# Kernel tuning notes

Hardware: AMD Instinct MI355X
Metric: run time of the kernel (lower is better)

## Reference

```python
import jax, jax.numpy as jnp
import numpy as np

N_NODES, N_EDGES, NNZ, F_IN, HID, K = 50000, 10000, 800000, 128, 512, 10


def setup_inputs() -> dict:
    key = jax.random.key(0)
    ks = jax.random.split(key, 6)
    x = jax.random.normal(ks[0], (N_NODES, F_IN), dtype=jnp.float32)
    node_idx = jax.random.randint(ks[1], (NNZ,), 0, N_NODES)
    edge_idx = jax.random.randint(ks[2], (NNZ,), 0, N_EDGES)
    hyperedge_index = jnp.stack([node_idx, edge_idx]).astype(jnp.int64)
    edge_weight = jax.random.uniform(ks[3], (N_EDGES,), dtype=jnp.float32, minval=0.5, maxval=1.5)
    theta = jax.random.normal(ks[4], (K + 1,), dtype=jnp.float32) * 0.1
    lin1_w = jax.random.normal(ks[5], (HID, F_IN), dtype=jnp.float32) * (1.0 / np.sqrt(F_IN))
    lin1_b = jnp.zeros((HID,), dtype=jnp.float32)
    return {"x": x, "hyperedge_index": hyperedge_index, "edge_weight": edge_weight,
            "theta": theta, "lin1_w": lin1_w, "lin1_b": lin1_b}


def _hyper_prop_factory(node_idx, edge_idx, edge_weight, n_nodes, n_edges):
    """Returns A_norm @ x where A_norm = Dv^-1/2 H W De^-1 H^T Dv^-1/2."""
    ones = jnp.ones_like(node_idx, dtype=edge_weight.dtype)
    d_e = jax.ops.segment_sum(ones, edge_idx, num_segments=n_edges)            # edge degree
    d_v = jax.ops.segment_sum(edge_weight[edge_idx], node_idx, num_segments=n_nodes)
    dv_is = jnp.where(d_v > 0, jax.lax.rsqrt(jnp.maximum(d_v, 1e-12)), 0.0)
    de_w = edge_weight * jnp.where(d_e > 0, 1.0 / jnp.maximum(d_e, 1e-12), 0.0)

    def prop(x):
        xv = x * dv_is[:, None]                                               # [N, F]
        m_e = jax.ops.segment_sum(xv[node_idx], edge_idx, num_segments=n_edges)
        m_e = m_e * de_w[:, None]                                             # [E, F]
        out = jax.ops.segment_sum(m_e[edge_idx], node_idx, num_segments=n_nodes)
        return out * dv_is[:, None]

    return prop


def cheb_hypergraph(x, node_idx, edge_idx, edge_weight, theta, n_nodes, n_edges):
    # L_tilde = L - I = -A_norm (lambda_max = 2). Chebyshev recurrence on L_tilde.
    prop = _hyper_prop_factory(node_idx, edge_idx, edge_weight, n_nodes, n_edges)
    t_prev = x                       # T_0
    out = theta[0] * t_prev
    t_cur = -prop(x)                 # T_1 = L_tilde x
    out = out + theta[1] * t_cur
    for k in range(2, theta.shape[0]):
        t_next = -2.0 * prop(t_cur) - t_prev   # T_k = 2 L_tilde T_{k-1} - T_{k-2}
        out = out + theta[k] * t_next
        t_prev, t_cur = t_cur, t_next
    return out


def reference(x, hyperedge_index, edge_weight, theta, lin1_w, lin1_b):
    node_idx = hyperedge_index[0]
    edge_idx = hyperedge_index[1]
    n_nodes = x.shape[0]
    n_edges = edge_weight.shape[0]
    # eval mode: both dropouts are identity
    h = cheb_hypergraph(x, node_idx, edge_idx, edge_weight, theta, n_nodes, n_edges)
    h = jnp.einsum('nf,hf->nh', h, lin1_w) + lin1_b
    # is_bns=False -> no batch norm; act_fn='relu'
    return jax.nn.relu(h)
```

## Files before the change

### kernel.cpp

```cpp
#include <hip/hip_runtime.h>


#define N_NODES 50000
#define N_EDGES 10000
#define NNZ     800000
#define F_IN    128
#define HID     512
#define F4      (F_IN / 4)
#define R16     16
#define NB_E    10
#define NB_N    49

typedef __attribute__((ext_vector_type(8))) short bf16x8;
typedef __attribute__((ext_vector_type(4))) float f32x4;

static __device__ __forceinline__ unsigned short f2bf(float f) {
    union { float f; unsigned u; } c; c.f = f;
    unsigned u = c.u;
    unsigned r = (u + 0x7fffu + ((u >> 16) & 1u)) >> 16;
    return (unsigned short)r;
}
static __device__ __forceinline__ float blo(unsigned u) {
    union { unsigned u; float f; } c; c.u = u << 16; return c.f;
}
static __device__ __forceinline__ float bhi(unsigned u) {
    union { unsigned u; float f; } c; c.u = u & 0xffff0000u; return c.f;
}
static __device__ __forceinline__ unsigned pack2(float lo, float hi) {
    return (unsigned)f2bf(lo) | ((unsigned)f2bf(hi) << 16);
}

__global__ void k_zero8(int* __restrict__ cnt8_e, int* __restrict__ cnt8_n) {
    int i = blockIdx.x * blockDim.x + threadIdx.x;
    if (i < 8 * N_NODES) cnt8_n[i] = 0;
    if (i < 8 * N_EDGES) cnt8_e[i] = 0;
}

__global__ void k_degrees(const int* __restrict__ hidx,
                          int* __restrict__ cnt8_e,
                          int* __restrict__ cnt8_n,
                          int* __restrict__ rank_e,
                          int* __restrict__ rank_v) {
    int i = blockIdx.x * blockDim.x + threadIdx.x;
    if (i >= NNZ) return;
    int xcd = (int)blockIdx.x & 7;
    int v = hidx[i];
    int e = hidx[NNZ + i];
    v = min(max(v, 0), N_NODES - 1);
    e = min(max(e, 0), N_EDGES - 1);
    int re = atomicAdd(&cnt8_e[xcd * N_EDGES + e], 1);
    int rv = atomicAdd(&cnt8_n[xcd * N_NODES + v], 1);
    rank_e[i] = re | (xcd << 24);
    rank_v[i] = rv | (xcd << 24);
}

__global__ void k_off8(int* __restrict__ cnt8_e,
                       int* __restrict__ cnt8_n,
                       int* __restrict__ counts_e,
                       int* __restrict__ counts_n) {
    int i = blockIdx.x * blockDim.x + threadIdx.x;
    if (i < N_EDGES) {
        int s = 0;
#pragma unroll
        for (int x = 0; x < 8; ++x) {
            int c = cnt8_e[x * N_EDGES + i];
            cnt8_e[x * N_EDGES + i] = s;
            s += c;
        }
        counts_e[i] = s;
    }
    if (i < N_NODES) {
        int s = 0;
#pragma unroll
        for (int x = 0; x < 8; ++x) {
            int c = cnt8_n[x * N_NODES + i];
            cnt8_n[x * N_NODES + i] = s;
            s += c;
        }
        counts_n[i] = s;
    }
}

__global__ __launch_bounds__(1024) void k_scan_blk2(const int* __restrict__ ce,
                                                    const int* __restrict__ cn,
                                                    int* __restrict__ oute,
                                                    int* __restrict__ outn,
                                                    int* __restrict__ pe,
                                                    int* __restrict__ pn) {
    __shared__ int sd[1024];
    int b = (int)blockIdx.x;
    const int* counts; int n; int* out; int* partial; int lb;
    if (b < NB_E) { counts = ce; n = N_EDGES; out = oute; partial = pe; lb = b; }
    else          { counts = cn; n = N_NODES; out = outn; partial = pn; lb = b - NB_E; }
    int tid = (int)threadIdx.x;
    int i = lb * 1024 + tid;
    int v = (i < n) ? counts[i] : 0;
    sd[tid] = v;
    __syncthreads();
    for (int off = 1; off < 1024; off <<= 1) {
        int t = (tid >= off) ? sd[tid - off] : 0;
        __syncthreads();
        sd[tid] += t;
        __syncthreads();
    }
    if (i < n) out[i] = sd[tid] - v;
    if (tid == 1023) partial[lb] = sd[1023];
}

__global__ void k_scan_top2(int* __restrict__ pe, int* __restrict__ pn,
                            int* __restrict__ tot_e, int* __restrict__ tot_n) {
    int w = (int)threadIdx.x >> 6;
    int lane = (int)threadIdx.x & 63;
    int* partial = w ? pn : pe;
    int nb       = w ? NB_N : NB_E;
    int* total   = w ? tot_n : tot_e;
    int v = (lane < nb) ? partial[lane] : 0;
    int incl = v;
    for (int off = 1; off < 64; off <<= 1) {
        int t = __shfl_up(incl, off);
        if (lane >= off) incl += t;
    }
    if (lane < nb) partial[lane] = incl - v;
    if (lane == 63) *total = incl;
}

__global__ __launch_bounds__(1024) void k_scan_add2(int* __restrict__ oute,
                                                    int* __restrict__ outn,
                                                    const int* __restrict__ pe,
                                                    const int* __restrict__ pn) {
    int b = (int)blockIdx.x;
    int* out; const int* partial; int n; int lb;
    if (b < NB_E) { out = oute; partial = pe; n = N_EDGES; lb = b; }
    else          { out = outn; partial = pn; n = N_NODES; lb = b - NB_E; }
    int i = lb * 1024 + (int)threadIdx.x;
    if (i < n) out[i] += partial[lb];
}

__global__ void k_fill(const int* __restrict__ hidx,
                       const int* __restrict__ edge_ptr,
                       const int* __restrict__ node_ptr,
                       const int* __restrict__ rank_e,
                       const int* __restrict__ rank_v,
                       const int* __restrict__ off8_e,
                       const int* __restrict__ off8_n,
                       int* __restrict__ edge_node,
                       int* __restrict__ node_edge) {
    int i = blockIdx.x * blockDim.x + threadIdx.x;
    if (i >= NNZ) return;
    int v = hidx[i];
    int e = hidx[NNZ + i];
    v = min(max(v, 0), N_NODES - 1);
    e = min(max(e, 0), N_EDGES - 1);
    int pe = rank_e[i];
    int pv = rank_v[i];
    int xe = pe >> 24, re = pe & 0xFFFFFF;
    int xv = pv >> 24, rv = pv & 0xFFFFFF;
    edge_node[edge_ptr[e] + off8_e[xe * N_EDGES + e] + re] = v;
    node_edge[node_ptr[v] + off8_n[xv * N_NODES + v] + rv] = e;
}

__global__ void k_norms2(const float* __restrict__ ew,
                         const int* __restrict__ edge_ptr,
                         const int* __restrict__ node_ptr,
                         const int* __restrict__ node_edge,
                         float* __restrict__ dv_is,
                         float* __restrict__ de_w) {
    int i = blockIdx.x * blockDim.x + threadIdx.x;
    if (i < N_NODES) {
        int s = node_ptr[i], t = node_ptr[i + 1];
        float d = 0.f;
        for (int j = s; j < t; ++j) d += ew[node_edge[j]];
        dv_is[i] = (d > 0.f) ? rsqrtf(fmaxf(d, 1e-12f)) : 0.f;
    }
    if (i < N_EDGES) {
        int c = edge_ptr[i + 1] - edge_ptr[i];
        de_w[i] = ew[i] * ((c > 0) ? (1.f / (float)c) : 0.f);
    }
}

__global__ void k_init(const float* __restrict__ x,
                       const float* __restrict__ theta,
                       const float* __restrict__ dv_is,
                       uint4* __restrict__ bufA,
                       float* __restrict__ acc) {
    int i = blockIdx.x * blockDim.x + threadIdx.x;
    if (i >= N_NODES * R16) return;
    int v = i >> 4;
    float dvv = dv_is[v];
    float w = (dvv > 0.f) ? dvv : 1.f;
    float4 x0 = ((const float4*)x)[2 * i];
    float4 x1 = ((const float4*)x)[2 * i + 1];
    uint4 q;
    q.x = pack2(w * x0.x, w * x0.y); q.y = pack2(w * x0.z, w * x0.w);
    q.z = pack2(w * x1.x, w * x1.y); q.w = pack2(w * x1.z, w * x1.w);
    bufA[i] = q;
    float t0 = theta[0];
    float4 a0, a1;
    a0.x = t0 * x0.x; a0.y = t0 * x0.y; a0.z = t0 * x0.z; a0.w = t0 * x0.w;
    a1.x = t0 * x1.x; a1.y = t0 * x1.y; a1.z = t0 * x1.z; a1.w = t0 * x1.w;
    ((float4*)acc)[2 * i]     = a0;
    ((float4*)acc)[2 * i + 1] = a1;
}

__global__ void k_phaseA(const uint4* __restrict__ tin,
                         const float* __restrict__ de_w,
                         const int* __restrict__ edge_ptr,
                         const int* __restrict__ edge_node,
                         uint4* __restrict__ m_e) {
    int tid    = (int)threadIdx.x;
    int g      = tid >> 6;
    int l64    = tid & 63;
    int stream = l64 >> 4;
    int lane   = l64 & 15;
    int e = blockIdx.x * 4 + g;
    int s = edge_ptr[e], t = edge_ptr[e + 1];
    float a0=0.f,a1=0.f,a2=0.f,a3=0.f,a4=0.f,a5=0.f,a6=0.f,a7=0.f;
    int j = s + stream;
    for (; j + 12 < t; j += 16) {
        int v0 = edge_node[j];
        int v1 = edge_node[j + 4];
        int v2 = edge_node[j + 8];
        int v3 = edge_node[j + 12];
        uint4 q0 = tin[v0 * R16 + lane];
        uint4 q1 = tin[v1 * R16 + lane];
        uint4 q2 = tin[v2 * R16 + lane];
        uint4 q3 = tin[v3 * R16 + lane];
        a0 += (blo(q0.x) + blo(q1.x)) + (blo(q2.x) + blo(q3.x));
        a1 += (bhi(q0.x) + bhi(q1.x)) + (bhi(q2.x) + bhi(q3.x));
        a2 += (blo(q0.y) + blo(q1.y)) + (blo(q2.y) + blo(q3.y));
        a3 += (bhi(q0.y) + bhi(q1.y)) + (bhi(q2.y) + bhi(q3.y));
        a4 += (blo(q0.z) + blo(q1.z)) + (blo(q2.z) + blo(q3.z));
        a5 += (bhi(q0.z) + bhi(q1.z)) + (bhi(q2.z) + bhi(q3.z));
        a6 += (blo(q0.w) + blo(q1.w)) + (blo(q2.w) + blo(q3.w));
        a7 += (bhi(q0.w) + bhi(q1.w)) + (bhi(q2.w) + bhi(q3.w));
    }
    for (; j < t; j += 4) {
        int v0 = edge_node[j];
        uint4 q0 = tin[v0 * R16 + lane];
        a0 += blo(q0.x); a1 += bhi(q0.x);
        a2 += blo(q0.y); a3 += bhi(q0.y);
        a4 += blo(q0.z); a5 += bhi(q0.z);
        a6 += blo(q0.w); a7 += bhi(q0.w);
    }
    a0 += __shfl_xor(a0, 16); a1 += __shfl_xor(a1, 16);
    a2 += __shfl_xor(a2, 16); a3 += __shfl_xor(a3, 16);
    a4 += __shfl_xor(a4, 16); a5 += __shfl_xor(a5, 16);
    a6 += __shfl_xor(a6, 16); a7 += __shfl_xor(a7, 16);
    a0 += __shfl_xor(a0, 32); a1 += __shfl_xor(a1, 32);
    a2 += __shfl_xor(a2, 32); a3 += __shfl_xor(a3, 32);
    a4 += __shfl_xor(a4, 32); a5 += __shfl_xor(a5, 32);
    a6 += __shfl_xor(a6, 32); a7 += __shfl_xor(a7, 32);
    if (stream == 0) {
        float w = de_w[e];
        uint4 o;
        o.x = pack2(a0 * w, a1 * w); o.y = pack2(a2 * w, a3 * w);
        o.z = pack2(a4 * w, a5 * w); o.w = pack2(a6 * w, a7 * w);
        m_e[e * R16 + lane] = o;
    }
}

__global__ void k_phaseB(const uint4* __restrict__ m_e,
                         const uint4* __restrict__ tin,
                         const float* __restrict__ dv_is,
                         const int* __restrict__ node_ptr,
                         const int* __restrict__ node_edge,
                         uint4* __restrict__ tio,
                         float* __restrict__ acc,
                         const float* __restrict__ theta, int k,
                         float ca, float cb, int accMode) {
    int g      = threadIdx.x >> 5;
    int stream = (threadIdx.x >> 4) & 1;
    int lane   = threadIdx.x & 15;
    int v = blockIdx.x * 8 + g;
    int s = node_ptr[v], t = node_ptr[v + 1];
    float s0=0.f,s1=0.f,s2=0.f,s3=0.f,s4=0.f,s5=0.f,s6=0.f,s7=0.f;
    int j = s + stream;
    for (; j + 2 < t; j += 4) {
        int e0 = node_edge[j];
        int e1 = node_edge[j + 2];
        uint4 q0 = m_e[e0 * R16 + lane];
        uint4 q1 = m_e[e1 * R16 + lane];
        s0 += blo(q0.x) + blo(q1.x); s1 += bhi(q0.x) + bhi(q1.x);
        s2 += blo(q0.y) + blo(q1.y); s3 += bhi(q0.y) + bhi(q1.y);
        s4 += blo(q0.z) + blo(q1.z); s5 += bhi(q0.z) + bhi(q1.z);
        s6 += blo(q0.w) + blo(q1.w); s7 += bhi(q0.w) + bhi(q1.w);
    }
    if (j < t) {
        int e0 = node_edge[j];
        uint4 q0 = m_e[e0 * R16 + lane];
        s0 += blo(q0.x); s1 += bhi(q0.x);
        s2 += blo(q0.y); s3 += bhi(q0.y);
        s4 += blo(q0.z); s5 += bhi(q0.z);
        s6 += blo(q0.w); s7 += bhi(q0.w);
    }
    s0 += __shfl_xor(s0, 16); s1 += __shfl_xor(s1, 16);
    s2 += __shfl_xor(s2, 16); s3 += __shfl_xor(s3, 16);
    s4 += __shfl_xor(s4, 16); s5 += __shfl_xor(s5, 16);
    s6 += __shfl_xor(s6, 16); s7 += __shfl_xor(s7, 16);
    if (stream == 0) {
        float dvv = dv_is[v];
        float scf = ca * dvv * dvv;
        int idx = v * R16 + lane;
        uint4 tp = tio[idx];
        float t0 = scf * s0 + cb * blo(tp.x);
        float t1 = scf * s1 + cb * bhi(tp.x);
        float t2 = scf * s2 + cb * blo(tp.y);
        float t3 = scf * s3 + cb * bhi(tp.y);
        float t4 = scf * s4 + cb * blo(tp.z);
        float t5 = scf * s5 + cb * bhi(tp.z);
        float t6 = scf * s6 + cb * blo(tp.w);
        float t7 = scf * s7 + cb * bhi(tp.w);
        uint4 tn;
        tn.x = pack2(t0, t1); tn.y = pack2(t2, t3);
        tn.z = pack2(t4, t5); tn.w = pack2(t6, t7);
        tio[idx] = tn;
        if (accMode) {
            float thk = theta[k];
            float a0 = thk * t0, a1 = thk * t1, a2 = thk * t2, a3 = thk * t3;
            float a4 = thk * t4, a5 = thk * t5, a6 = thk * t6, a7 = thk * t7;
            if (accMode >= 2) {
                float th1 = theta[k - 1];
                uint4 tq = tin[idx];
                a0 += th1 * blo(tq.x); a1 += th1 * bhi(tq.x);
                a2 += th1 * blo(tq.y); a3 += th1 * bhi(tq.y);
                a4 += th1 * blo(tq.z); a5 += th1 * bhi(tq.z);
                a6 += th1 * blo(tq.w); a7 += th1 * bhi(tq.w);
            }
            if (accMode >= 3) {
                float th2 = theta[k - 2];
                a0 += th2 * blo(tp.x); a1 += th2 * bhi(tp.x);
                a2 += th2 * blo(tp.y); a3 += th2 * bhi(tp.y);
                a4 += th2 * blo(tp.z); a5 += th2 * bhi(tp.z);
                a6 += th2 * blo(tp.w); a7 += th2 * bhi(tp.w);
            }
            float iw = (dvv > 0.f) ? (1.f / dvv) : 1.f;
            float4* acc4 = (float4*)acc;
            int ai = v * 32 + lane * 2;
            float4 a = acc4[ai];
            a.x += iw * a0; a.y += iw * a1; a.z += iw * a2; a.w += iw * a3;
            acc4[ai] = a;
            float4 b = acc4[ai + 1];
            b.x += iw * a4; b.y += iw * a5; b.z += iw * a6; b.w += iw * a7;
            acc4[ai + 1] = b;
        }
    }
}

#define M_TILES 782
__global__ __launch_bounds__(256) void k_gemm(const float* __restrict__ A,
                                              const float* __restrict__ W,
                                              const float* __restrict__ bias,
                                              float* __restrict__ out) {
    __shared__ short Asm[64 * 136];
    __shared__ short Wsm[64 * 136];
    int id  = (int)blockIdx.x;
    int xcd = id & 7;
    int sub = id >> 3;
    int h_t = sub & 7;
    int m_i = sub >> 3;
    int m_t = xcd * 98 + m_i;
    if (m_t >= M_TILES) return;
    int m0 = m_t * 64;
    int h0 = h_t * 64;
    int tid = (int)threadIdx.x;

    const float4* A4 = (const float4*)A;
    const float4* W4 = (const float4*)W;
#pragma unroll
    for (int i = 0; i < 4; ++i) {
        int c   = tid + i * 256;
        int row = c >> 4;
        int q4  = c & 15;
        int gr = m0 + row;
        float4 a0, a1;
        if (gr < N_NODES) {
            a0 = A4[(size_t)gr * 32 + q4 * 2];
            a1 = A4[(size_t)gr * 32 + q4 * 2 + 1];
        } else {
            a0 = make_float4(0.f, 0.f, 0.f, 0.f);
            a1 = a0;
        }
        uint4 pa;
        pa.x = pack2(a0.x, a0.y); pa.y = pack2(a0.z, a0.w);
        pa.z = pack2(a1.x, a1.y); pa.w = pack2(a1.z, a1.w);
        *(uint4*)&Asm[row * 136 + q4 * 8] = pa;
        float4 w0 = W4[(size_t)(h0 + row) * 32 + q4 * 2];
        float4 w1 = W4[(size_t)(h0 + row) * 32 + q4 * 2 + 1];
        uint4 pw;
        pw.x = pack2(w0.x, w0.y); pw.y = pack2(w0.z, w0.w);
        pw.z = pack2(w1.x, w1.y); pw.w = pack2(w1.z, w1.w);
        *(uint4*)&Wsm[row * 136 + q4 * 8] = pw;
    }
    __syncthreads();

    int lane = tid & 63;
    int wv   = tid >> 6;
    int l16  = lane & 15;
    int quad = lane >> 4;

    f32x4 acc[4];
#pragma unroll
    for (int n = 0; n < 4; ++n) acc[n] = (f32x4){0.f, 0.f, 0.f, 0.f};

#pragma unroll
    for (int ks = 0; ks < 4; ++ks) {
        int k0 = ks * 32;
        bf16x8 af = *(const bf16x8*)&Asm[(wv * 16 + l16) * 136 + k0 + quad * 8];
#pragma unroll
        for (int n = 0; n < 4; ++n) {
            bf16x8 bf = *(const bf16x8*)&Wsm[(n * 16 + l16) * 136 + k0 + quad * 8];
            acc[n] = __builtin_amdgcn_mfma_f32_16x16x32_bf16(af, bf, acc[n], 0, 0, 0);
        }
    }

#pragma unroll
    for (int n = 0; n < 4; ++n) {
        float bb = bias[h0 + n * 16 + l16];
#pragma unroll
        for (int r = 0; r < 4; ++r) {
            int gr = m0 + wv * 16 + quad * 4 + r;
            if (gr < N_NODES)
                out[(size_t)gr * HID + h0 + n * 16 + l16] =
                    fmaxf(acc[n][r] + bb, 0.f);
        }
    }
}

extern "C" void kernel_launch(void* const* d_in, const int* in_sizes, int n_in,
                              void* d_out, int out_size, void* d_ws, size_t ws_size,
                              hipStream_t stream) {
    const float* x     = (const float*)d_in[0];
    const int*   hidx  = (const int*)d_in[1];
    const float* ew    = (const float*)d_in[2];
    const float* theta = (const float*)d_in[3];
    const float* w1    = (const float*)d_in[4];
    const float* b1    = (const float*)d_in[5];
    float*       out   = (float*)d_out;
    int kp1 = in_sizes[3];
    int K   = kp1 - 1;

    char* ob = (char*)d_out;
    size_t oo = 0;
    auto oalloc = [&](size_t bytes) -> void* {
        void* p = ob + oo;
        oo = (oo + bytes + 255) & ~(size_t)255;
        return p;
    };
    uint4* bufA      = (uint4*)oalloc((size_t)N_NODES * F_IN * 2);
    uint4* bufB      = (uint4*)oalloc((size_t)N_NODES * F_IN * 2);
    uint4* m_e       = (uint4*)oalloc((size_t)N_EDGES * F_IN * 2);
    int*   edge_node = (int*)oalloc((size_t)NNZ * 4);
    int*   node_edge = (int*)oalloc((size_t)NNZ * 4);
    int*   rank_e    = (int*)oalloc((size_t)NNZ * 4);
    int*   rank_v    = (int*)oalloc((size_t)NNZ * 4);
    int*   cnt8_e    = (int*)oalloc((size_t)8 * N_EDGES * 4);
    int*   cnt8_n    = (int*)oalloc((size_t)8 * N_NODES * 4);
    int*   counts_e  = (int*)oalloc((size_t)N_EDGES * 4);
    int*   counts_n  = (int*)oalloc((size_t)N_NODES * 4);

    char* ws = (char*)d_ws;
    size_t off = 0;
    auto alloc = [&](size_t bytes) -> void* {
        void* p = ws + off;
        off = (off + bytes + 255) & ~(size_t)255;
        return p;
    };
    float* accv     = (float*)alloc((size_t)N_NODES * F_IN * 4);
    float* dv_is    = (float*)alloc((size_t)N_NODES * 4);
    float* de_w     = (float*)alloc((size_t)N_EDGES * 4);
    int*   edge_ptr = (int*)alloc((size_t)(N_EDGES + 1) * 4);
    int*   node_ptr = (int*)alloc((size_t)(N_NODES + 1) * 4);
    int*   part_e   = (int*)alloc(64 * 4);
    int*   part_n   = (int*)alloc(64 * 4);

    k_zero8<<<(8 * N_NODES + 255) / 256, 256, 0, stream>>>(cnt8_e, cnt8_n);
    k_degrees<<<(NNZ + 255) / 256, 256, 0, stream>>>(hidx, cnt8_e, cnt8_n, rank_e, rank_v);
    k_off8<<<(N_NODES + 255) / 256, 256, 0, stream>>>(cnt8_e, cnt8_n, counts_e, counts_n);

    k_scan_blk2<<<NB_E + NB_N, 1024, 0, stream>>>(counts_e, counts_n, edge_ptr, node_ptr,
                                                  part_e, part_n);
    k_scan_top2<<<1, 128, 0, stream>>>(part_e, part_n, edge_ptr + N_EDGES, node_ptr + N_NODES);
    k_scan_add2<<<NB_E + NB_N, 1024, 0, stream>>>(edge_ptr, node_ptr, part_e, part_n);

    k_fill<<<(NNZ + 255) / 256, 256, 0, stream>>>(hidx, edge_ptr, node_ptr,
                                                  rank_e, rank_v, cnt8_e, cnt8_n,
                                                  edge_node, node_edge);
    k_norms2<<<(N_NODES + 255) / 256, 256, 0, stream>>>(ew, edge_ptr, node_ptr,
                                                        node_edge, dv_is, de_w);
    k_init<<<(N_NODES * R16 + 255) / 256, 256, 0, stream>>>(x, theta, dv_is, bufA, accv);

    for (int k = 1; k <= K; ++k) {
        const uint4* tin = (k & 1) ? bufA : bufB;
        uint4*       tio = (k & 1) ? bufB : bufA;
        float ca = (k == 1) ? -1.f : -2.f;
        float cb = (k == 1) ? 0.f : -1.f;
        int accMode = 0;
        if (k % 3 == 0) accMode = 3;
        else if (k == K && (K % 3) != 0) accMode = K % 3;
        k_phaseA<<<N_EDGES / 4, 256, 0, stream>>>(tin, de_w, edge_ptr, edge_node, m_e);
        k_phaseB<<<N_NODES / 8, 256, 0, stream>>>(m_e, tin, dv_is, node_ptr, node_edge,
                                                  tio, accv, theta, k, ca, cb, accMode);
    }

    k_gemm<<<8 * 98 * 8, 256, 0, stream>>>(accv, w1, b1, out);
}
```

Before: 774.2 us.

## Build CSR with per-block LDS histograms instead of global atomics

Replaces the global-atomic counting sort (8 XCD-sliced counters plus zeroing kernel) with 64 workgroups that each build packed 16-bit node and edge histograms in LDS. A combine kernel turns these into per-block base offsets, and fill uses block-local ranks stored as ushort. This removes global atomic contention and the zero kernel, but adds a 64-way serial combine pass and large LDS use (about 120 KB) that limits each block to low occupancy.

```diff
diff --git a/kernel.cpp b/kernel.cpp
--- a/kernel.cpp
+++ b/kernel.cpp
@@ -10,6 +10,9 @@
 #define R16     16
 #define NB_E    10
 #define NB_N    49
+#define HB      64
+#define NW_E    (N_EDGES / 2)
+#define NW_N    (N_NODES / 2)
 
 typedef __attribute__((ext_vector_type(8))) short bf16x8;
 typedef __attribute__((ext_vector_type(4))) float f32x4;
@@ -30,52 +33,61 @@
     return (unsigned)f2bf(lo) | ((unsigned)f2bf(hi) << 16);
 }
 
-__global__ void k_zero8(int* __restrict__ cnt8_e, int* __restrict__ cnt8_n) {
-    int i = blockIdx.x * blockDim.x + threadIdx.x;
-    if (i < 8 * N_NODES) cnt8_n[i] = 0;
-    if (i < 8 * N_EDGES) cnt8_e[i] = 0;
-}
-
-__global__ void k_degrees(const int* __restrict__ hidx,
-                          int* __restrict__ cnt8_e,
-                          int* __restrict__ cnt8_n,
-                          int* __restrict__ rank_e,
-                          int* __restrict__ rank_v) {
-    int i = blockIdx.x * blockDim.x + threadIdx.x;
-    if (i >= NNZ) return;
-    int xcd = (int)blockIdx.x & 7;
-    int v = hidx[i];
-    int e = hidx[NNZ + i];
-    v = min(max(v, 0), N_NODES - 1);
-    e = min(max(e, 0), N_EDGES - 1);
-    int re = atomicAdd(&cnt8_e[xcd * N_EDGES + e], 1);
-    int rv = atomicAdd(&cnt8_n[xcd * N_NODES + v], 1);
-    rank_e[i] = re | (xcd << 24);
-    rank_v[i] = rv | (xcd << 24);
-}
-
-__global__ void k_off8(int* __restrict__ cnt8_e,
-                       int* __restrict__ cnt8_n,
-                       int* __restrict__ counts_e,
-                       int* __restrict__ counts_n) {
+__global__ __launch_bounds__(1024) void k_hist(const int* __restrict__ hidx,
+                                               unsigned short* __restrict__ loc_e,
+                                               unsigned short* __restrict__ loc_v,
+                                               unsigned* __restrict__ hist_e,
+                                               unsigned* __restrict__ hist_n) {
+    __shared__ unsigned she[NW_E];
+    __shared__ unsigned shn[NW_N];
+    int tid = (int)threadIdx.x;
+    for (int w = tid; w < NW_E; w += 1024) she[w] = 0;
+    for (int w = tid; w < NW_N; w += 1024) shn[w] = 0;
+    __syncthreads();
+    int bid = (int)blockIdx.x;
+    for (int i = bid * 1024 + tid; i < NNZ; i += HB * 1024) {
+        int v = hidx[i];
+        int e = hidx[NNZ + i];
+        v = min(max(v, 0), N_NODES - 1);
+        e = min(max(e, 0), N_EDGES - 1);
+        int se = (e & 1) * 16;
+        int sv = (v & 1) * 16;
+        unsigned oe = atomicAdd(&she[e >> 1], 1u << se);
+        unsigned ov = atomicAdd(&shn[v >> 1], 1u << sv);
+        loc_e[i] = (unsigned short)((oe >> se) & 0xFFFFu);
+        loc_v[i] = (unsigned short)((ov >> sv) & 0xFFFFu);
+    }
+    __syncthreads();
+    for (int w = tid; w < NW_E; w += 1024) hist_e[bid * NW_E + w] = she[w];
+    for (int w = tid; w < NW_N; w += 1024) hist_n[bid * NW_N + w] = shn[w];
+}
+
+__global__ void k_combine(const unsigned* __restrict__ hist_e,
+                          const unsigned* __restrict__ hist_n,
+                          int* __restrict__ base_e,
+                          int* __restrict__ base_n,
+                          int* __restrict__ counts_e,
+                          int* __restrict__ counts_n) {
     int i = blockIdx.x * blockDim.x + threadIdx.x;
     if (i < N_EDGES) {
+        int sh = (i & 1) * 16;
+        int w = i >> 1;
         int s = 0;
-#pragma unroll
-        for (int x = 0; x < 8; ++x) {
-            int c = cnt8_e[x * N_EDGES + i];
-            cnt8_e[x * N_EDGES + i] = s;
-            s += c;
+#pragma unroll 8
+        for (int b = 0; b < HB; ++b) {
+            base_e[b * N_EDGES + i] = s;
+            s += (int)((hist_e[b * NW_E + w] >> sh) & 0xFFFFu);
         }
         counts_e[i] = s;
     }
     if (i < N_NODES) {
+        int sh = (i & 1) * 16;
+        int w = i >> 1;
         int s = 0;
-#pragma unroll
-        for (int x = 0; x < 8; ++x) {
-            int c = cnt8_n[x * N_NODES + i];
-            cnt8_n[x * N_NODES + i] = s;
-            s += c;
+#pragma unroll 8
+        for (int b = 0; b < HB; ++b) {
+            base_n[b * N_NODES + i] = s;
+            s += (int)((hist_n[b * NW_N + w] >> sh) & 0xFFFFu);
         }
         counts_n[i] = s;
     }
@@ -139,24 +151,21 @@
 __global__ void k_fill(const int* __restrict__ hidx,
                        const int* __restrict__ edge_ptr,
                        const int* __restrict__ node_ptr,
-                       const int* __restrict__ rank_e,
-                       const int* __restrict__ rank_v,
-                       const int* __restrict__ off8_e,
-                       const int* __restrict__ off8_n,
+                       const unsigned short* __restrict__ loc_e,
+                       const unsigned short* __restrict__ loc_v,
+                       const int* __restrict__ base_e,
+                       const int* __restrict__ base_n,
                        int* __restrict__ edge_node,
                        int* __restrict__ node_edge) {
     int i = blockIdx.x * blockDim.x + threadIdx.x;
     if (i >= NNZ) return;
+    int wg = (i >> 10) & (HB - 1);
     int v = hidx[i];
     int e = hidx[NNZ + i];
     v = min(max(v, 0), N_NODES - 1);
     e = min(max(e, 0), N_EDGES - 1);
-    int pe = rank_e[i];
-    int pv = rank_v[i];
-    int xe = pe >> 24, re = pe & 0xFFFFFF;
-    int xv = pv >> 24, rv = pv & 0xFFFFFF;
-    edge_node[edge_ptr[e] + off8_e[xe * N_EDGES + e] + re] = v;
-    node_edge[node_ptr[v] + off8_n[xv * N_NODES + v] + rv] = e;
+    edge_node[edge_ptr[e] + base_e[wg * N_EDGES + e] + (int)loc_e[i]] = v;
+    node_edge[node_ptr[v] + base_n[wg * N_NODES + v] + (int)loc_v[i]] = e;
 }
 
 __global__ void k_norms2(const float* __restrict__ ew,
@@ -451,10 +460,12 @@
     uint4* m_e       = (uint4*)oalloc((size_t)N_EDGES * F_IN * 2);
     int*   edge_node = (int*)oalloc((size_t)NNZ * 4);
     int*   node_edge = (int*)oalloc((size_t)NNZ * 4);
-    int*   rank_e    = (int*)oalloc((size_t)NNZ * 4);
-    int*   rank_v    = (int*)oalloc((size_t)NNZ * 4);
-    int*   cnt8_e    = (int*)oalloc((size_t)8 * N_EDGES * 4);
-    int*   cnt8_n    = (int*)oalloc((size_t)8 * N_NODES * 4);
+    unsigned short* loc_e = (unsigned short*)oalloc((size_t)NNZ * 2);
+    unsigned short* loc_v = (unsigned short*)oalloc((size_t)NNZ * 2);
+    unsigned* hist_e = (unsigned*)oalloc((size_t)HB * NW_E * 4);
+    unsigned* hist_n = (unsigned*)oalloc((size_t)HB * NW_N * 4);
+    int*   base_e    = (int*)oalloc((size_t)HB * N_EDGES * 4);
+    int*   base_n    = (int*)oalloc((size_t)HB * N_NODES * 4);
     int*   counts_e  = (int*)oalloc((size_t)N_EDGES * 4);
     int*   counts_n  = (int*)oalloc((size_t)N_NODES * 4);
 
@@ -473,9 +484,10 @@
     int*   part_e   = (int*)alloc(64 * 4);
     int*   part_n   = (int*)alloc(64 * 4);
 
-    k_zero8<<<(8 * N_NODES + 255) / 256, 256, 0, stream>>>(cnt8_e, cnt8_n);
-    k_degrees<<<(NNZ + 255) / 256, 256, 0, stream>>>(hidx, cnt8_e, cnt8_n, rank_e, rank_v);
-    k_off8<<<(N_NODES + 255) / 256, 256, 0, stream>>>(cnt8_e, cnt8_n, counts_e, counts_n);
+    k_hist<<<HB, 1024, 0, stream>>>(hidx, loc_e, loc_v, hist_e, hist_n);
+    k_combine<<<(N_NODES + 255) / 256, 256, 0, stream>>>(hist_e, hist_n,
+                                                         base_e, base_n,
+                                                         counts_e, counts_n);
 
     k_scan_blk2<<<NB_E + NB_N, 1024, 0, stream>>>(counts_e, counts_n, edge_ptr, node_ptr,
                                                   part_e, part_n);
@@ -483,7 +495,7 @@
     k_scan_add2<<<NB_E + NB_N, 1024, 0, stream>>>(edge_ptr, node_ptr, part_e, part_n);
 
     k_fill<<<(NNZ + 255) / 256, 256, 0, stream>>>(hidx, edge_ptr, node_ptr,
-                                                  rank_e, rank_v, cnt8_e, cnt8_n,
+                                                  loc_e, loc_v, base_e, base_n,
                                                   edge_node, node_edge);
     k_norms2<<<(N_NODES + 255) / 256, 256, 0, stream>>>(ew, edge_ptr, node_ptr,
                                                         node_edge, dv_is, de_w);
```

Result: faster. 745.4 us (-3.7%).
